# Performance work log

Hardware: AMD Instinct MI355X
Metric: run time of the kernel (lower is better)

Reference implementation:

```python
import jax, jax.numpy as jnp
import numpy as np

N_USERS = 50000
N_ENTITIES = 100000
N_RELATIONS = 16
N_EDGES = 3200000
NNZ = 2500000
CH = 64
N_HOPS = 2


def l2_normalize(x, eps=1e-12):
    # matches torch F.normalize(dim=1): x / max(||x||_2, eps)
    n = jnp.sqrt(jnp.sum(x * x, axis=-1, keepdims=True))
    return x / jnp.maximum(n, eps)


def setup_inputs() -> dict:
    key = jax.random.key(0)
    ks = jax.random.split(key, 10)
    user_emb = jax.random.normal(ks[0], (N_USERS, CH), dtype=jnp.float32)
    entity_emb = jax.random.normal(ks[1], (N_ENTITIES, CH), dtype=jnp.float32)
    weight = jax.random.normal(ks[2], (N_RELATIONS, CH), dtype=jnp.float32)
    triplet_mask = jax.random.uniform(ks[3], (N_EDGES,), dtype=jnp.float32)
    interact_vals = jnp.ones((NNZ,), dtype=jnp.float32)
    edge_head = jax.random.randint(ks[4], (N_EDGES,), 0, N_ENTITIES, dtype=jnp.int32)
    edge_tail = jax.random.randint(ks[5], (N_EDGES,), 0, N_ENTITIES, dtype=jnp.int32)
    edge_type = jax.random.randint(ks[6], (N_EDGES,), 1, N_RELATIONS + 1, dtype=jnp.int32)
    interact_rows = jax.random.randint(ks[7], (NNZ,), 0, N_USERS, dtype=jnp.int32)
    interact_cols = jax.random.randint(ks[8], (NNZ,), 0, N_ENTITIES, dtype=jnp.int32)
    return {
        'user_emb': user_emb, 'entity_emb': entity_emb, 'weight': weight,
        'triplet_mask': triplet_mask, 'interact_vals': interact_vals,
        'edge_head': edge_head, 'edge_tail': edge_tail, 'edge_type': edge_type,
        'interact_rows': interact_rows, 'interact_cols': interact_cols,
    }


def reference(user_emb, entity_emb, weight, triplet_mask, interact_vals,
              edge_head, edge_tail, edge_type, interact_rows, interact_cols):
    unmask = triplet_mask
    entity_res = entity_emb
    user_res = user_emb
    for _ in range(N_HOPS):
        # KG aggregate: gather tail embeddings, mask + relation multiply, scatter-sum to heads
        neigh = entity_emb[edge_tail] * unmask[:, None] * weight[edge_type - 1]  # [E, CH]
        entity_agg = jax.ops.segment_sum(neigh, edge_head, num_segments=N_ENTITIES)
        # user aggregate: sparse interact_mat @ entity_emb (COO gather + segment_sum)
        user_agg = jax.ops.segment_sum(
            interact_vals[:, None] * entity_emb[interact_cols],
            interact_rows, num_segments=N_USERS)
        # mess_dropout disabled (eval mode -> identity)
        entity_emb = l2_normalize(entity_agg)
        user_emb = l2_normalize(user_agg)
        entity_res = entity_res + entity_emb
        user_res = user_res + user_emb
    return entity_res, user_res
```

## Files before the change

kernel.cpp:

```cpp
#include <hip/hip_runtime.h>

#define N_USERS 50000
#define N_ENTITIES 100000
#define N_RELATIONS 16
#define N_EDGES 3200000
#define NNZ 2500000
#define CH 64

#define RPB 64
#define NB_E 1563
#define NB_U 782
#define CAP_E 2560
#define CAP_U 3840

#define BKG 128
#define BU  96
#define BTOT (BKG + BU)

__device__ __forceinline__ unsigned short f2bf(float f) {
    unsigned u = __float_as_uint(f);
    u += 0x7FFF + ((u >> 16) & 1);
    return (unsigned short)(u >> 16);
}

__global__ void __launch_bounds__(1024)
build_kernel(const float4* __restrict__ user_emb,
             const float4* __restrict__ entity_emb,
             ushort4* __restrict__ cur_bf,
             float4* __restrict__ out_entity,
             float4* __restrict__ out_user,
             const int* __restrict__ head, const int* __restrict__ tail,
             const int* __restrict__ type, const float* __restrict__ maskp,
             const int* __restrict__ irows, const int* __restrict__ icols,
             const float* __restrict__ ivals,
             int* __restrict__ cntE, int2* __restrict__ binE,
             int* __restrict__ cntU, int2* __restrict__ binU) {
    __shared__ int hist[NB_E];
    __shared__ int lbase[NB_E];
    const int blk = blockIdx.x;
    const int t = threadIdx.x;

    if (blk >= BTOT) {
        const int ne4 = N_ENTITIES * CH / 4;
        const int nu4 = N_USERS * CH / 4;
        int i = (blk - BTOT) * 1024 + t;
        if (i < ne4) {
            float4 v = entity_emb[i];
            out_entity[i] = v;
            ushort4 bq;
            bq.x = f2bf(v.x); bq.y = f2bf(v.y); bq.z = f2bf(v.z); bq.w = f2bf(v.w);
            cur_bf[i] = bq;
        }
        if (i < nu4) out_user[i] = user_emb[i];
        return;
    }

    if (blk < BKG) {
        for (int i = t; i < NB_E; i += 1024) hist[i] = 0;
        __syncthreads();
        const int chunk = (N_EDGES + BKG - 1) / BKG;
        int base = blk * chunk;
        int lim = min(base + chunk, N_EDGES);
        for (int i = base + t; i < lim; i += 1024)
            atomicAdd(&hist[head[i] >> 6], 1);
        __syncthreads();
        for (int i = t; i < NB_E; i += 1024) {
            int c = hist[i];
            lbase[i] = c ? atomicAdd(&cntE[i], c) : 0;
            hist[i] = 0;
        }
        __syncthreads();
        int i = base + t;
        for (; i + 3072 < lim; i += 4096) {
            int i0 = i, i1 = i + 1024, i2 = i + 2048, i3 = i + 3072;
            int h0 = head[i0], h1 = head[i1], h2 = head[i2], h3 = head[i3];
            int k0 = tail[i0] | ((type[i0] - 1) << 17) | ((h0 & 63) << 21);
            int k1 = tail[i1] | ((type[i1] - 1) << 17) | ((h1 & 63) << 21);
            int k2 = tail[i2] | ((type[i2] - 1) << 17) | ((h2 & 63) << 21);
            int k3 = tail[i3] | ((type[i3] - 1) << 17) | ((h3 & 63) << 21);
            float m0 = maskp[i0], m1 = maskp[i1], m2 = maskp[i2], m3 = maskp[i3];
            int b0 = h0 >> 6, b1 = h1 >> 6, b2 = h2 >> 6, b3 = h3 >> 6;
            int l0 = lbase[b0] + atomicAdd(&hist[b0], 1);
            int l1 = lbase[b1] + atomicAdd(&hist[b1], 1);
            int l2 = lbase[b2] + atomicAdd(&hist[b2], 1);
            int l3 = lbase[b3] + atomicAdd(&hist[b3], 1);
            if (l0 < CAP_E) binE[(size_t)b0 * CAP_E + l0] = make_int2(k0, __float_as_int(m0));
            if (l1 < CAP_E) binE[(size_t)b1 * CAP_E + l1] = make_int2(k1, __float_as_int(m1));
            if (l2 < CAP_E) binE[(size_t)b2 * CAP_E + l2] = make_int2(k2, __float_as_int(m2));
            if (l3 < CAP_E) binE[(size_t)b3 * CAP_E + l3] = make_int2(k3, __float_as_int(m3));
        }
        for (; i < lim; i += 1024) {
            int h = head[i];
            int b = h >> 6;
            int loc = lbase[b] + atomicAdd(&hist[b], 1);
            if (loc < CAP_E)
                binE[(size_t)b * CAP_E + loc] =
                    make_int2(tail[i] | ((type[i] - 1) << 17) | ((h & 63) << 21),
                              __float_as_int(maskp[i]));
        }
    } else {
        const int ub = blk - BKG;
        for (int i = t; i < NB_U; i += 1024) hist[i] = 0;
        __syncthreads();
        const int chunk = (NNZ + BU - 1) / BU;
        int base = ub * chunk;
        int lim = min(base + chunk, NNZ);
        for (int i = base + t; i < lim; i += 1024)
            atomicAdd(&hist[irows[i] >> 6], 1);
        __syncthreads();
        for (int i = t; i < NB_U; i += 1024) {
            int c = hist[i];
            lbase[i] = c ? atomicAdd(&cntU[i], c) : 0;
            hist[i] = 0;
        }
        __syncthreads();
        int i = base + t;
        for (; i + 3072 < lim; i += 4096) {
            int i0 = i, i1 = i + 1024, i2 = i + 2048, i3 = i + 3072;
            int r0 = irows[i0], r1 = irows[i1], r2 = irows[i2], r3 = irows[i3];
            int k0 = icols[i0] | ((r0 & 63) << 17);
            int k1 = icols[i1] | ((r1 & 63) << 17);
            int k2 = icols[i2] | ((r2 & 63) << 17);
            int k3 = icols[i3] | ((r3 & 63) << 17);
            float v0 = ivals[i0], v1 = ivals[i1], v2 = ivals[i2], v3 = ivals[i3];
            int b0 = r0 >> 6, b1 = r1 >> 6, b2 = r2 >> 6, b3 = r3 >> 6;
            int l0 = lbase[b0] + atomicAdd(&hist[b0], 1);
            int l1 = lbase[b1] + atomicAdd(&hist[b1], 1);
            int l2 = lbase[b2] + atomicAdd(&hist[b2], 1);
            int l3 = lbase[b3] + atomicAdd(&hist[b3], 1);
            if (l0 < CAP_U) binU[(size_t)b0 * CAP_U + l0] = make_int2(k0, __float_as_int(v0));
            if (l1 < CAP_U) binU[(size_t)b1 * CAP_U + l1] = make_int2(k1, __float_as_int(v1));
            if (l2 < CAP_U) binU[(size_t)b2 * CAP_U + l2] = make_int2(k2, __float_as_int(v2));
            if (l3 < CAP_U) binU[(size_t)b3 * CAP_U + l3] = make_int2(k3, __float_as_int(v3));
        }
        for (; i < lim; i += 1024) {
            int r = irows[i];
            int b = r >> 6;
            int loc = lbase[b] + atomicAdd(&hist[b], 1);
            if (loc < CAP_U)
                binU[(size_t)b * CAP_U + loc] =
                    make_int2(icols[i] | ((r & 63) << 17), __float_as_int(ivals[i]));
        }
    }
}

__global__ void __launch_bounds__(512)
sort_kernel(int2* __restrict__ binE, const int* __restrict__ cntE,
            int2* __restrict__ binU, const int* __restrict__ cntU,
            int* __restrict__ rowptr) {
    __shared__ int2 buf[CAP_U];
    __shared__ int2 sbuf[CAP_U];
    __shared__ int  hist[RPB];
    __shared__ int  offs[RPB + 1];

    const int b = blockIdx.x;
    const int t = threadIdx.x;
    const bool is_user = (b < NB_U);
    const int eb = b - NB_U;
    int2* __restrict__ bin = is_user ? (binU + (size_t)b * CAP_U)
                                     : (binE + (size_t)eb * CAP_E);
    const int cnt = is_user ? min(cntU[b], CAP_U) : min(cntE[eb], CAP_E);
    const int rsh = is_user ? 17 : 21;

    if (t < RPB) hist[t] = 0;
    for (int i = t; i < cnt; i += 512) buf[i] = bin[i];
    __syncthreads();
    for (int i = t; i < cnt; i += 512)
        atomicAdd(&hist[(buf[i].x >> rsh) & 63], 1);
    __syncthreads();
    if (t < 64) {
        int v = hist[t];
        int s = v;
        #pragma unroll
        for (int d = 1; d < 64; d <<= 1) {
            int nb = __shfl_up(s, d, 64);
            if (t >= d) s += nb;
        }
        offs[t] = s - v;
        if (t == 63) offs[64] = s;
    }
    __syncthreads();
    if (t < RPB) hist[t] = 0;
    __syncthreads();
    for (int i = t; i < cnt; i += 512) {
        int2 p = buf[i];
        int r = (p.x >> rsh) & 63;
        int k = atomicAdd(&hist[r], 1);
        sbuf[offs[r] + k] = p;
    }
    __syncthreads();
    for (int i = t; i < cnt; i += 512) bin[i] = sbuf[i];
    if (t <= 64) rowptr[b * 65 + t] = offs[t];
}

__global__ void __launch_bounds__(512)
agg_kernel(const uint2* __restrict__ cur64,
           const float* __restrict__ weight,
           const int2* __restrict__ binE, const int2* __restrict__ binU,
           const int* __restrict__ rowptr,
           unsigned short* __restrict__ nxt,
           float* __restrict__ res_e, float* __restrict__ res_u) {
    __shared__ float4 wl4[N_RELATIONS * 16];
    __shared__ int    srp[RPB + 1];

    const int b = blockIdx.x;
    const int t = threadIdx.x;
    const int w = t >> 6;
    const int lane = t & 63;
    const int g = lane >> 4;
    const int c2 = lane & 15;
    const bool is_user = (b < NB_U);
    const int eb = b - NB_U;
    const int2* __restrict__ bin = is_user ? (binU + (size_t)b * CAP_U)
                                           : (binE + (size_t)eb * CAP_E);

    if (!is_user)
        for (int i = t; i < N_RELATIONS * 16; i += 512)
            wl4[i] = ((const float4*)weight)[i];
    if (t < RPB + 1) srp[t] = rowptr[b * 65 + t];
    __syncthreads();

    #pragma unroll
    for (int rr = 0; rr < 8; ++rr) {
        const int row = (w << 3) + rr;
        const int s = srp[row], e = srp[row + 1];
        float x0 = 0.f, x1 = 0.f, x2 = 0.f, x3 = 0.f;
        int i = s;
        if (is_user) {
            for (; i + 7 < e; i += 8) {
                int2 pa = bin[i + g];
                int2 pb = bin[i + 4 + g];
                uint2 qa = cur64[(size_t)(pa.x & 0x1FFFF) * 16 + c2];
                uint2 qb = cur64[(size_t)(pb.x & 0x1FFFF) * 16 + c2];
                float sa = __int_as_float(pa.y);
                float sb = __int_as_float(pb.y);
                x0 += __uint_as_float(qa.x << 16) * sa;
                x1 += __uint_as_float(qa.x & 0xFFFF0000u) * sa;
                x2 += __uint_as_float(qa.y << 16) * sa;
                x3 += __uint_as_float(qa.y & 0xFFFF0000u) * sa;
                x0 += __uint_as_float(qb.x << 16) * sb;
                x1 += __uint_as_float(qb.x & 0xFFFF0000u) * sb;
                x2 += __uint_as_float(qb.y << 16) * sb;
                x3 += __uint_as_float(qb.y & 0xFFFF0000u) * sb;
            }
            for (; i < e; i += 4) {
                int idx = i + g;
                bool vld = idx < e;
                int2 p = bin[vld ? idx : i];
                uint2 q = cur64[(size_t)(p.x & 0x1FFFF) * 16 + c2];
                float sv = vld ? __int_as_float(p.y) : 0.f;
                x0 += __uint_as_float(q.x << 16) * sv;
                x1 += __uint_as_float(q.x & 0xFFFF0000u) * sv;
                x2 += __uint_as_float(q.y << 16) * sv;
                x3 += __uint_as_float(q.y & 0xFFFF0000u) * sv;
            }
        } else {
            for (; i + 7 < e; i += 8) {
                int2 pa = bin[i + g];
                int2 pb = bin[i + 4 + g];
                uint2 qa = cur64[(size_t)(pa.x & 0x1FFFF) * 16 + c2];
                uint2 qb = cur64[(size_t)(pb.x & 0x1FFFF) * 16 + c2];
                float4 wa = wl4[((pa.x >> 17) & 15) * 16 + c2];
                float4 wb = wl4[((pb.x >> 17) & 15) * 16 + c2];
                float sa = __int_as_float(pa.y);
                float sb = __int_as_float(pb.y);
                x0 += __uint_as_float(qa.x << 16) * (sa * wa.x);
                x1 += __uint_as_float(qa.x & 0xFFFF0000u) * (sa * wa.y);
                x2 += __uint_as_float(qa.y << 16) * (sa * wa.z);
                x3 += __uint_as_float(qa.y & 0xFFFF0000u) * (sa * wa.w);
                x0 += __uint_as_float(qb.x << 16) * (sb * wb.x);
                x1 += __uint_as_float(qb.x & 0xFFFF0000u) * (sb * wb.y);
                x2 += __uint_as_float(qb.y << 16) * (sb * wb.z);
                x3 += __uint_as_float(qb.y & 0xFFFF0000u) * (sb * wb.w);
            }
            for (; i < e; i += 4) {
                int idx = i + g;
                bool vld = idx < e;
                int2 p = bin[vld ? idx : i];
                uint2 q = cur64[(size_t)(p.x & 0x1FFFF) * 16 + c2];
                float4 wv = wl4[((p.x >> 17) & 15) * 16 + c2];
                float sv = vld ? __int_as_float(p.y) : 0.f;
                x0 += __uint_as_float(q.x << 16) * (sv * wv.x);
                x1 += __uint_as_float(q.x & 0xFFFF0000u) * (sv * wv.y);
                x2 += __uint_as_float(q.y << 16) * (sv * wv.z);
                x3 += __uint_as_float(q.y & 0xFFFF0000u) * (sv * wv.w);
            }
        }

        x0 += __shfl_xor(x0, 16, 64); x0 += __shfl_xor(x0, 32, 64);
        x1 += __shfl_xor(x1, 16, 64); x1 += __shfl_xor(x1, 32, 64);
        x2 += __shfl_xor(x2, 16, 64); x2 += __shfl_xor(x2, 32, 64);
        x3 += __shfl_xor(x3, 16, 64); x3 += __shfl_xor(x3, 32, 64);
        float ss = x0 * x0 + x1 * x1 + x2 * x2 + x3 * x3;
        #pragma unroll
        for (int o = 8; o; o >>= 1) ss += __shfl_xor(ss, o, 64);
        float inv = 1.f / fmaxf(sqrtf(ss), 1e-12f);
        float y0 = x0 * inv, y1 = x1 * inv, y2 = x2 * inv, y3 = x3 * inv;
        if (g == 0) {
            if (is_user) {
                int grow = b * RPB + row;
                if (grow < N_USERS) {
                    float4* p = (float4*)res_u + (size_t)grow * 16 + c2;
                    float4 v = *p;
                    v.x += y0; v.y += y1; v.z += y2; v.w += y3;
                    *p = v;
                }
            } else {
                int grow = eb * RPB + row;
                if (grow < N_ENTITIES) {
                    uint2 pk;
                    pk.x = (unsigned)f2bf(y0) | ((unsigned)f2bf(y1) << 16);
                    pk.y = (unsigned)f2bf(y2) | ((unsigned)f2bf(y3) << 16);
                    ((uint2*)nxt)[(size_t)grow * 16 + c2] = pk;
                    float4* p = (float4*)res_e + (size_t)grow * 16 + c2;
                    float4 v = *p;
                    v.x += y0; v.y += y1; v.z += y2; v.w += y3;
                    *p = v;
                }
            }
        }
    }
}

extern "C" void kernel_launch(void* const* d_in, const int* in_sizes, int n_in,
                              void* d_out, int out_size, void* d_ws, size_t ws_size,
                              hipStream_t stream) {
    const float* user_emb   = (const float*)d_in[0];
    const float* entity_emb = (const float*)d_in[1];
    const float* weight     = (const float*)d_in[2];
    const float* mask       = (const float*)d_in[3];
    const float* ivals      = (const float*)d_in[4];
    const int*   edge_head  = (const int*)d_in[5];
    const int*   edge_tail  = (const int*)d_in[6];
    const int*   edge_type  = (const int*)d_in[7];
    const int*   irows      = (const int*)d_in[8];
    const int*   icols      = (const int*)d_in[9];

    float* out_entity = (float*)d_out;
    float* out_user   = (float*)d_out + (size_t)N_ENTITIES * CH;

    unsigned short* curA = (unsigned short*)d_ws;
    unsigned short* curB = curA + (size_t)N_ENTITIES * CH;
    int2* binE = (int2*)(curB + (size_t)N_ENTITIES * CH);
    int2* binU = binE + (size_t)NB_E * CAP_E;
    int*  cntE = (int*)(binU + (size_t)NB_U * CAP_U);
    int*  cntU = cntE + NB_E;
    int*  rowptr = cntU + NB_U;

    hipMemsetAsync(cntE, 0, (size_t)(NB_E + NB_U) * sizeof(int), stream);
    {
        const int init_blocks = (N_ENTITIES * CH / 4 + 1023) / 1024;
        build_kernel<<<BTOT + init_blocks, 1024, 0, stream>>>(
            (const float4*)user_emb, (const float4*)entity_emb,
            (ushort4*)curA, (float4*)out_entity, (float4*)out_user,
            edge_head, edge_tail, edge_type, mask,
            irows, icols, ivals,
            cntE, binE, cntU, binU);
    }

    sort_kernel<<<NB_U + NB_E, 512, 0, stream>>>(binE, cntE, binU, cntU, rowptr);

    agg_kernel<<<NB_U + NB_E, 512, 0, stream>>>(
        (const uint2*)curA, weight, binE, binU, rowptr,
        curB, out_entity, out_user);
    agg_kernel<<<NB_U + NB_E, 512, 0, stream>>>(
        (const uint2*)curB, weight, binE, binU, rowptr,
        curA, out_entity, out_user);
}
```

Before: 550.7 us.

## Replace single-pass padded binning with two-level radix partition into compact bins

The one-pass scatter into 64-row padded bins, which uses shared histograms of up to 1563 entries and many scattered write targets, is replaced by a two-level partition. The first pass scatters into coarse 2048-row buckets, using the output buffer as scratch. A scan over the fine counts then sets offsets, and a second pass scatters into a compact contiguous array. This aims for more local writes and higher occupancy during binning, and removes the padding slack in later reads, at the cost of extra kernel launches and one more pass over the edge data.

```diff
diff --git a/kernel.cpp b/kernel.cpp
--- a/kernel.cpp
+++ b/kernel.cpp
@@ -10,12 +10,19 @@
 #define RPB 64
 #define NB_E 1563
 #define NB_U 782
-#define CAP_E 2560
-#define CAP_U 3840
-
-#define BKG 128
-#define BU  96
-#define BTOT (BKG + BU)
+#define NBUCKETS (NB_E + NB_U)
+#define STAGE 3840
+
+#define NCE 49
+#define NCU 25
+#define CAPC_E 67072
+#define CAPC_U 104448
+#define NCU_DOUT 14
+
+#define PA_KG 256
+#define PA_U  192
+#define SE 10
+#define SU 16
 
 __device__ __forceinline__ unsigned short f2bf(float f) {
     unsigned u = __float_as_uint(f);
@@ -23,27 +30,232 @@
     return (unsigned short)(u >> 16);
 }
 
+__device__ __forceinline__ int wave_incl_scan(int v, int lane) {
+    int s = v;
+    #pragma unroll
+    for (int d = 1; d < 64; d <<= 1) {
+        int x = __shfl_up(s, d, 64);
+        if (lane >= d) s += x;
+    }
+    return s;
+}
+
 __global__ void __launch_bounds__(1024)
-build_kernel(const float4* __restrict__ user_emb,
-             const float4* __restrict__ entity_emb,
-             ushort4* __restrict__ cur_bf,
-             float4* __restrict__ out_entity,
-             float4* __restrict__ out_user,
-             const int* __restrict__ head, const int* __restrict__ tail,
+passA_kernel(const int* __restrict__ head, const int* __restrict__ tail,
              const int* __restrict__ type, const float* __restrict__ maskp,
              const int* __restrict__ irows, const int* __restrict__ icols,
              const float* __restrict__ ivals,
-             int* __restrict__ cntE, int2* __restrict__ binE,
-             int* __restrict__ cntU, int2* __restrict__ binU) {
-    __shared__ int hist[NB_E];
-    __shared__ int lbase[NB_E];
+             int* __restrict__ fineCnt, int* __restrict__ cCurE,
+             int* __restrict__ cCurU,
+             int2* __restrict__ cbE, int2* __restrict__ cbU_d,
+             int2* __restrict__ cbU_w) {
+    __shared__ int histF[NB_E];
+    __shared__ int histC[64];
+    __shared__ int lbase[64];
+    __shared__ int2* utab[NCU];
     const int blk = blockIdx.x;
     const int t = threadIdx.x;
 
-    if (blk >= BTOT) {
+    if (blk < PA_KG) {
+        for (int i = t; i < NB_E; i += 1024) histF[i] = 0;
+        if (t < NCE) histC[t] = 0;
+        __syncthreads();
+        const int chunk = (N_EDGES + PA_KG - 1) / PA_KG;
+        int base = blk * chunk, lim = min(base + chunk, N_EDGES);
+        for (int i = base + t; i < lim; i += 1024) {
+            int h = head[i];
+            atomicAdd(&histF[h >> 6], 1);
+            atomicAdd(&histC[h >> 11], 1);
+        }
+        __syncthreads();
+        for (int i = t; i < NB_E; i += 1024)
+            if (histF[i]) atomicAdd(&fineCnt[NB_U + i], histF[i]);
+        if (t < NCE) {
+            int c = histC[t];
+            lbase[t] = c ? atomicAdd(&cCurE[t], c) : 0;
+            histC[t] = 0;
+        }
+        __syncthreads();
+        int i = base + t;
+        for (; i + 3072 < lim; i += 4096) {
+            int i0 = i, i1 = i + 1024, i2 = i + 2048, i3 = i + 3072;
+            int h0 = head[i0], h1 = head[i1], h2 = head[i2], h3 = head[i3];
+            int x0 = tail[i0] | ((type[i0] - 1) << 17) | ((h0 & 63) << 21) | (((h0 >> 6) & 31) << 27);
+            int x1 = tail[i1] | ((type[i1] - 1) << 17) | ((h1 & 63) << 21) | (((h1 >> 6) & 31) << 27);
+            int x2 = tail[i2] | ((type[i2] - 1) << 17) | ((h2 & 63) << 21) | (((h2 >> 6) & 31) << 27);
+            int x3 = tail[i3] | ((type[i3] - 1) << 17) | ((h3 & 63) << 21) | (((h3 >> 6) & 31) << 27);
+            float m0 = maskp[i0], m1 = maskp[i1], m2 = maskp[i2], m3 = maskp[i3];
+            int c0 = h0 >> 11, c1 = h1 >> 11, c2 = h2 >> 11, c3 = h3 >> 11;
+            int l0 = lbase[c0] + atomicAdd(&histC[c0], 1);
+            int l1 = lbase[c1] + atomicAdd(&histC[c1], 1);
+            int l2 = lbase[c2] + atomicAdd(&histC[c2], 1);
+            int l3 = lbase[c3] + atomicAdd(&histC[c3], 1);
+            if (l0 < CAPC_E) cbE[(size_t)c0 * CAPC_E + l0] = make_int2(x0, __float_as_int(m0));
+            if (l1 < CAPC_E) cbE[(size_t)c1 * CAPC_E + l1] = make_int2(x1, __float_as_int(m1));
+            if (l2 < CAPC_E) cbE[(size_t)c2 * CAPC_E + l2] = make_int2(x2, __float_as_int(m2));
+            if (l3 < CAPC_E) cbE[(size_t)c3 * CAPC_E + l3] = make_int2(x3, __float_as_int(m3));
+        }
+        for (; i < lim; i += 1024) {
+            int h = head[i];
+            int x = tail[i] | ((type[i] - 1) << 17) | ((h & 63) << 21) | (((h >> 6) & 31) << 27);
+            int c = h >> 11;
+            int loc = lbase[c] + atomicAdd(&histC[c], 1);
+            if (loc < CAPC_E)
+                cbE[(size_t)c * CAPC_E + loc] = make_int2(x, __float_as_int(maskp[i]));
+        }
+    } else {
+        if (t < NCU)
+            utab[t] = (t < NCU_DOUT) ? (cbU_d + (size_t)t * CAPC_U)
+                                     : (cbU_w + (size_t)(t - NCU_DOUT) * CAPC_U);
+        for (int i = t; i < NB_U; i += 1024) histF[i] = 0;
+        if (t < NCU) histC[t] = 0;
+        __syncthreads();
+        const int ub = blk - PA_KG;
+        const int chunk = (NNZ + PA_U - 1) / PA_U;
+        int base = ub * chunk, lim = min(base + chunk, NNZ);
+        for (int i = base + t; i < lim; i += 1024) {
+            int r = irows[i];
+            atomicAdd(&histF[r >> 6], 1);
+            atomicAdd(&histC[r >> 11], 1);
+        }
+        __syncthreads();
+        for (int i = t; i < NB_U; i += 1024)
+            if (histF[i]) atomicAdd(&fineCnt[i], histF[i]);
+        if (t < NCU) {
+            int c = histC[t];
+            lbase[t] = c ? atomicAdd(&cCurU[t], c) : 0;
+            histC[t] = 0;
+        }
+        __syncthreads();
+        int i = base + t;
+        for (; i + 3072 < lim; i += 4096) {
+            int i0 = i, i1 = i + 1024, i2 = i + 2048, i3 = i + 3072;
+            int r0 = irows[i0], r1 = irows[i1], r2 = irows[i2], r3 = irows[i3];
+            int x0 = icols[i0] | ((r0 & 63) << 17) | (((r0 >> 6) & 31) << 27);
+            int x1 = icols[i1] | ((r1 & 63) << 17) | (((r1 >> 6) & 31) << 27);
+            int x2 = icols[i2] | ((r2 & 63) << 17) | (((r2 >> 6) & 31) << 27);
+            int x3 = icols[i3] | ((r3 & 63) << 17) | (((r3 >> 6) & 31) << 27);
+            float v0 = ivals[i0], v1 = ivals[i1], v2 = ivals[i2], v3 = ivals[i3];
+            int c0 = r0 >> 11, c1 = r1 >> 11, c2 = r2 >> 11, c3 = r3 >> 11;
+            int l0 = lbase[c0] + atomicAdd(&histC[c0], 1);
+            int l1 = lbase[c1] + atomicAdd(&histC[c1], 1);
+            int l2 = lbase[c2] + atomicAdd(&histC[c2], 1);
+            int l3 = lbase[c3] + atomicAdd(&histC[c3], 1);
+            if (l0 < CAPC_U) utab[c0][l0] = make_int2(x0, __float_as_int(v0));
+            if (l1 < CAPC_U) utab[c1][l1] = make_int2(x1, __float_as_int(v1));
+            if (l2 < CAPC_U) utab[c2][l2] = make_int2(x2, __float_as_int(v2));
+            if (l3 < CAPC_U) utab[c3][l3] = make_int2(x3, __float_as_int(v3));
+        }
+        for (; i < lim; i += 1024) {
+            int r = irows[i];
+            int x = icols[i] | ((r & 63) << 17) | (((r >> 6) & 31) << 27);
+            int c = r >> 11;
+            int loc = lbase[c] + atomicAdd(&histC[c], 1);
+            if (loc < CAPC_U) utab[c][loc] = make_int2(x, __float_as_int(ivals[i]));
+        }
+    }
+}
+
+__global__ void __launch_bounds__(512)
+scan_kernel(const int* __restrict__ fineCnt, int* __restrict__ fineBase,
+            int* __restrict__ fineCur) {
+    __shared__ int wsums[8];
+    __shared__ int carry_s;
+    const int t = threadIdx.x, w = t >> 6, lane = t & 63;
+    if (t == 0) carry_s = 0;
+    __syncthreads();
+    for (int base = 0; base < NBUCKETS; base += 512) {
+        int i = base + t;
+        int v = (i < NBUCKETS) ? fineCnt[i] : 0;
+        int s = wave_incl_scan(v, lane);
+        if (lane == 63) wsums[w] = s;
+        __syncthreads();
+        int carry = carry_s;
+        if (w == 0) {
+            int ws = (lane < 8) ? wsums[lane] : 0;
+            int ss = wave_incl_scan(ws, lane);
+            if (lane < 8) wsums[lane] = ss - ws;
+        }
+        __syncthreads();
+        int excl = s - v + wsums[w] + carry;
+        if (i < NBUCKETS) { fineBase[i] = excl; fineCur[i] = excl; }
+        __syncthreads();
+        if (t == 511) carry_s = excl + v;
+        __syncthreads();
+    }
+}
+
+__global__ void __launch_bounds__(1024)
+passB_kernel(const int* __restrict__ cCurE, const int* __restrict__ cCurU,
+             const int2* __restrict__ cbE, const int2* __restrict__ cbU_d,
+             const int2* __restrict__ cbU_w,
+             int* __restrict__ fineCur, int2* __restrict__ binAll) {
+    __shared__ int h32[32];
+    __shared__ int lb[32];
+    const int blk = blockIdx.x, t = threadIdx.x;
+    const int2* __restrict__ src;
+    int cnt, sub, S, fid0;
+    if (blk < NCE * SE) {
+        int c = blk / SE; sub = blk % SE; S = SE;
+        cnt = min(cCurE[c], CAPC_E);
+        src = cbE + (size_t)c * CAPC_E;
+        fid0 = NB_U + c * 32;
+    } else {
+        int c = (blk - NCE * SE) / SU; sub = (blk - NCE * SE) % SU; S = SU;
+        cnt = min(cCurU[c], CAPC_U);
+        src = (c < NCU_DOUT) ? cbU_d + (size_t)c * CAPC_U
+                             : cbU_w + (size_t)(c - NCU_DOUT) * CAPC_U;
+        fid0 = c * 32;
+    }
+    int len = (cnt + S - 1) / S;
+    int b0 = sub * len, b1 = min(b0 + len, cnt);
+    if (t < 32) h32[t] = 0;
+    __syncthreads();
+    for (int i = b0 + t; i < b1; i += 1024)
+        atomicAdd(&h32[(src[i].x >> 27) & 31], 1);
+    __syncthreads();
+    if (t < 32) {
+        int c2 = h32[t];
+        lb[t] = c2 ? atomicAdd(&fineCur[fid0 + t], c2) : 0;
+        h32[t] = 0;
+    }
+    __syncthreads();
+    int i = b0 + t;
+    for (; i + 3072 < b1; i += 4096) {
+        int2 e0 = src[i], e1 = src[i + 1024], e2 = src[i + 2048], e3 = src[i + 3072];
+        int f0 = (e0.x >> 27) & 31, f1 = (e1.x >> 27) & 31;
+        int f2 = (e2.x >> 27) & 31, f3 = (e3.x >> 27) & 31;
+        int l0 = lb[f0] + atomicAdd(&h32[f0], 1);
+        int l1 = lb[f1] + atomicAdd(&h32[f1], 1);
+        int l2 = lb[f2] + atomicAdd(&h32[f2], 1);
+        int l3 = lb[f3] + atomicAdd(&h32[f3], 1);
+        binAll[l0] = e0; binAll[l1] = e1; binAll[l2] = e2; binAll[l3] = e3;
+    }
+    for (; i < b1; i += 1024) {
+        int2 e = src[i];
+        int f = (e.x >> 27) & 31;
+        binAll[lb[f] + atomicAdd(&h32[f], 1)] = e;
+    }
+}
+
+__global__ void __launch_bounds__(512)
+sortinit_kernel(int2* __restrict__ binAll, const int* __restrict__ fineCnt,
+                const int* __restrict__ fineBase, int* __restrict__ rowptr,
+                const float4* __restrict__ user_emb,
+                const float4* __restrict__ entity_emb,
+                ushort4* __restrict__ cur_bf,
+                float4* __restrict__ out_entity, float4* __restrict__ out_user) {
+    __shared__ int2 buf[STAGE];
+    __shared__ int2 sbuf[STAGE];
+    __shared__ int  hist[RPB];
+    __shared__ int  offs[RPB + 1];
+
+    const int blk = blockIdx.x;
+    const int t = threadIdx.x;
+    if (blk >= NBUCKETS) {
         const int ne4 = N_ENTITIES * CH / 4;
         const int nu4 = N_USERS * CH / 4;
-        int i = (blk - BTOT) * 1024 + t;
+        int i = (blk - NBUCKETS) * 512 + t;
         if (i < ne4) {
             float4 v = entity_emb[i];
             out_entity[i] = v;
@@ -55,111 +267,11 @@
         return;
     }
 
-    if (blk < BKG) {
-        for (int i = t; i < NB_E; i += 1024) hist[i] = 0;
-        __syncthreads();
-        const int chunk = (N_EDGES + BKG - 1) / BKG;
-        int base = blk * chunk;
-        int lim = min(base + chunk, N_EDGES);
-        for (int i = base + t; i < lim; i += 1024)
-            atomicAdd(&hist[head[i] >> 6], 1);
-        __syncthreads();
-        for (int i = t; i < NB_E; i += 1024) {
-            int c = hist[i];
-            lbase[i] = c ? atomicAdd(&cntE[i], c) : 0;
-            hist[i] = 0;
-        }
-        __syncthreads();
-        int i = base + t;
-        for (; i + 3072 < lim; i += 4096) {
-            int i0 = i, i1 = i + 1024, i2 = i + 2048, i3 = i + 3072;
-            int h0 = head[i0], h1 = head[i1], h2 = head[i2], h3 = head[i3];
-            int k0 = tail[i0] | ((type[i0] - 1) << 17) | ((h0 & 63) << 21);
-            int k1 = tail[i1] | ((type[i1] - 1) << 17) | ((h1 & 63) << 21);
-            int k2 = tail[i2] | ((type[i2] - 1) << 17) | ((h2 & 63) << 21);
-            int k3 = tail[i3] | ((type[i3] - 1) << 17) | ((h3 & 63) << 21);
-            float m0 = maskp[i0], m1 = maskp[i1], m2 = maskp[i2], m3 = maskp[i3];
-            int b0 = h0 >> 6, b1 = h1 >> 6, b2 = h2 >> 6, b3 = h3 >> 6;
-            int l0 = lbase[b0] + atomicAdd(&hist[b0], 1);
-            int l1 = lbase[b1] + atomicAdd(&hist[b1], 1);
-            int l2 = lbase[b2] + atomicAdd(&hist[b2], 1);
-            int l3 = lbase[b3] + atomicAdd(&hist[b3], 1);
-            if (l0 < CAP_E) binE[(size_t)b0 * CAP_E + l0] = make_int2(k0, __float_as_int(m0));
-            if (l1 < CAP_E) binE[(size_t)b1 * CAP_E + l1] = make_int2(k1, __float_as_int(m1));
-            if (l2 < CAP_E) binE[(size_t)b2 * CAP_E + l2] = make_int2(k2, __float_as_int(m2));
-            if (l3 < CAP_E) binE[(size_t)b3 * CAP_E + l3] = make_int2(k3, __float_as_int(m3));
-        }
-        for (; i < lim; i += 1024) {
-            int h = head[i];
-            int b = h >> 6;
-            int loc = lbase[b] + atomicAdd(&hist[b], 1);
-            if (loc < CAP_E)
-                binE[(size_t)b * CAP_E + loc] =
-                    make_int2(tail[i] | ((type[i] - 1) << 17) | ((h & 63) << 21),
-                              __float_as_int(maskp[i]));
-        }
-    } else {
-        const int ub = blk - BKG;
-        for (int i = t; i < NB_U; i += 1024) hist[i] = 0;
-        __syncthreads();
-        const int chunk = (NNZ + BU - 1) / BU;
-        int base = ub * chunk;
-        int lim = min(base + chunk, NNZ);
-        for (int i = base + t; i < lim; i += 1024)
-            atomicAdd(&hist[irows[i] >> 6], 1);
-        __syncthreads();
-        for (int i = t; i < NB_U; i += 1024) {
-            int c = hist[i];
-            lbase[i] = c ? atomicAdd(&cntU[i], c) : 0;
-            hist[i] = 0;
-        }
-        __syncthreads();
-        int i = base + t;
-        for (; i + 3072 < lim; i += 4096) {
-            int i0 = i, i1 = i + 1024, i2 = i + 2048, i3 = i + 3072;
-            int r0 = irows[i0], r1 = irows[i1], r2 = irows[i2], r3 = irows[i3];
-            int k0 = icols[i0] | ((r0 & 63) << 17);
-            int k1 = icols[i1] | ((r1 & 63) << 17);
-            int k2 = icols[i2] | ((r2 & 63) << 17);
-            int k3 = icols[i3] | ((r3 & 63) << 17);
-            float v0 = ivals[i0], v1 = ivals[i1], v2 = ivals[i2], v3 = ivals[i3];
-            int b0 = r0 >> 6, b1 = r1 >> 6, b2 = r2 >> 6, b3 = r3 >> 6;
-            int l0 = lbase[b0] + atomicAdd(&hist[b0], 1);
-            int l1 = lbase[b1] + atomicAdd(&hist[b1], 1);
-            int l2 = lbase[b2] + atomicAdd(&hist[b2], 1);
-            int l3 = lbase[b3] + atomicAdd(&hist[b3], 1);
-            if (l0 < CAP_U) binU[(size_t)b0 * CAP_U + l0] = make_int2(k0, __float_as_int(v0));
-            if (l1 < CAP_U) binU[(size_t)b1 * CAP_U + l1] = make_int2(k1, __float_as_int(v1));
-            if (l2 < CAP_U) binU[(size_t)b2 * CAP_U + l2] = make_int2(k2, __float_as_int(v2));
-            if (l3 < CAP_U) binU[(size_t)b3 * CAP_U + l3] = make_int2(k3, __float_as_int(v3));
-        }
-        for (; i < lim; i += 1024) {
-            int r = irows[i];
-            int b = r >> 6;
-            int loc = lbase[b] + atomicAdd(&hist[b], 1);
-            if (loc < CAP_U)
-                binU[(size_t)b * CAP_U + loc] =
-                    make_int2(icols[i] | ((r & 63) << 17), __float_as_int(ivals[i]));
-        }
-    }
-}
-
-__global__ void __launch_bounds__(512)
-sort_kernel(int2* __restrict__ binE, const int* __restrict__ cntE,
-            int2* __restrict__ binU, const int* __restrict__ cntU,
-            int* __restrict__ rowptr) {
-    __shared__ int2 buf[CAP_U];
-    __shared__ int2 sbuf[CAP_U];
-    __shared__ int  hist[RPB];
-    __shared__ int  offs[RPB + 1];
-
-    const int b = blockIdx.x;
-    const int t = threadIdx.x;
+    const int b = blk;
     const bool is_user = (b < NB_U);
-    const int eb = b - NB_U;
-    int2* __restrict__ bin = is_user ? (binU + (size_t)b * CAP_U)
-                                     : (binE + (size_t)eb * CAP_E);
-    const int cnt = is_user ? min(cntU[b], CAP_U) : min(cntE[eb], CAP_E);
+    const int base = fineBase[b];
+    int2* __restrict__ bin = binAll + base;
+    const int cnt = min(fineCnt[b], STAGE);
     const int rsh = is_user ? 17 : 21;
 
     if (t < RPB) hist[t] = 0;
@@ -170,12 +282,7 @@
     __syncthreads();
     if (t < 64) {
         int v = hist[t];
-        int s = v;
-        #pragma unroll
-        for (int d = 1; d < 64; d <<= 1) {
-            int nb = __shfl_up(s, d, 64);
-            if (t >= d) s += nb;
-        }
+        int s = wave_incl_scan(v, t);
         offs[t] = s - v;
         if (t == 63) offs[64] = s;
     }
@@ -190,14 +297,13 @@
     }
     __syncthreads();
     for (int i = t; i < cnt; i += 512) bin[i] = sbuf[i];
-    if (t <= 64) rowptr[b * 65 + t] = offs[t];
+    if (t <= 64) rowptr[b * 65 + t] = base + offs[t];
 }
 
 __global__ void __launch_bounds__(512)
 agg_kernel(const uint2* __restrict__ cur64,
            const float* __restrict__ weight,
-           const int2* __restrict__ binE, const int2* __restrict__ binU,
-           const int* __restrict__ rowptr,
+           const int2* __restrict__ binAll, const int* __restrict__ rowptr,
            unsigned short* __restrict__ nxt,
            float* __restrict__ res_e, float* __restrict__ res_u) {
     __shared__ float4 wl4[N_RELATIONS * 16];
@@ -211,8 +317,6 @@
     const int c2 = lane & 15;
     const bool is_user = (b < NB_U);
     const int eb = b - NB_U;
-    const int2* __restrict__ bin = is_user ? (binU + (size_t)b * CAP_U)
-                                           : (binE + (size_t)eb * CAP_E);
 
     if (!is_user)
         for (int i = t; i < N_RELATIONS * 16; i += 512)
@@ -228,8 +332,8 @@
         int i = s;
         if (is_user) {
             for (; i + 7 < e; i += 8) {
-                int2 pa = bin[i + g];
-                int2 pb = bin[i + 4 + g];
+                int2 pa = binAll[i + g];
+                int2 pb = binAll[i + 4 + g];
                 uint2 qa = cur64[(size_t)(pa.x & 0x1FFFF) * 16 + c2];
                 uint2 qb = cur64[(size_t)(pb.x & 0x1FFFF) * 16 + c2];
                 float sa = __int_as_float(pa.y);
@@ -246,7 +350,7 @@
             for (; i < e; i += 4) {
                 int idx = i + g;
                 bool vld = idx < e;
-                int2 p = bin[vld ? idx : i];
+                int2 p = binAll[vld ? idx : i];
                 uint2 q = cur64[(size_t)(p.x & 0x1FFFF) * 16 + c2];
                 float sv = vld ? __int_as_float(p.y) : 0.f;
                 x0 += __uint_as_float(q.x << 16) * sv;
@@ -256,8 +360,8 @@
             }
         } else {
             for (; i + 7 < e; i += 8) {
-                int2 pa = bin[i + g];
-                int2 pb = bin[i + 4 + g];
+                int2 pa = binAll[i + g];
+                int2 pb = binAll[i + 4 + g];
                 uint2 qa = cur64[(size_t)(pa.x & 0x1FFFF) * 16 + c2];
                 uint2 qb = cur64[(size_t)(pb.x & 0x1FFFF) * 16 + c2];
                 float4 wa = wl4[((pa.x >> 17) & 15) * 16 + c2];
@@ -276,7 +380,7 @@
             for (; i < e; i += 4) {
                 int idx = i + g;
                 bool vld = idx < e;
-                int2 p = bin[vld ? idx : i];
+                int2 p = binAll[vld ? idx : i];
                 uint2 q = cur64[(size_t)(p.x & 0x1FFFF) * 16 + c2];
                 float4 wv = wl4[((p.x >> 17) & 15) * 16 + c2];
                 float sv = vld ? __int_as_float(p.y) : 0.f;
@@ -339,31 +443,43 @@
     float* out_entity = (float*)d_out;
     float* out_user   = (float*)d_out + (size_t)N_ENTITIES * CH;
 
+    int2* cbE   = (int2*)d_out;
+    int2* cbU_d = cbE + (size_t)NCE * CAPC_E;
+
     unsigned short* curA = (unsigned short*)d_ws;
     unsigned short* curB = curA + (size_t)N_ENTITIES * CH;
-    int2* binE = (int2*)(curB + (size_t)N_ENTITIES * CH);
-    int2* binU = binE + (size_t)NB_E * CAP_E;
-    int*  cntE = (int*)(binU + (size_t)NB_U * CAP_U);
-    int*  cntU = cntE + NB_E;
-    int*  rowptr = cntU + NB_U;
-
-    hipMemsetAsync(cntE, 0, (size_t)(NB_E + NB_U) * sizeof(int), stream);
+    int2* binAll = (int2*)(curB + (size_t)N_ENTITIES * CH);
+    int2* cbU_w  = binAll + (size_t)(N_EDGES + NNZ);
+    int*  fineCnt  = (int*)(cbU_w + (size_t)(NCU - NCU_DOUT) * CAPC_U);
+    int*  cCurE    = fineCnt + NBUCKETS;
+    int*  cCurU    = cCurE + NCE;
+    int*  fineBase = cCurU + NCU;
+    int*  fineCur  = fineBase + NBUCKETS;
+    int*  rowptr   = fineCur + NBUCKETS;
+
+    hipMemsetAsync(fineCnt, 0, (size_t)(NBUCKETS + NCE + NCU) * sizeof(int), stream);
+
+    passA_kernel<<<PA_KG + PA_U, 1024, 0, stream>>>(
+        edge_head, edge_tail, edge_type, mask, irows, icols, ivals,
+        fineCnt, cCurE, cCurU, cbE, cbU_d, cbU_w);
+
+    scan_kernel<<<1, 512, 0, stream>>>(fineCnt, fineBase, fineCur);
+
+    passB_kernel<<<NCE * SE + NCU * SU, 1024, 0, stream>>>(
+        cCurE, cCurU, cbE, cbU_d, cbU_w, fineCur, binAll);
+
     {
-        const int init_blocks = (N_ENTITIES * CH / 4 + 1023) / 1024;
-        build_kernel<<<BTOT + init_blocks, 1024, 0, stream>>>(
+        const int init_blocks = (N_ENTITIES * CH / 4 + 511) / 512;
+        sortinit_kernel<<<NBUCKETS + init_blocks, 512, 0, stream>>>(
+            binAll, fineCnt, fineBase, rowptr,
             (const float4*)user_emb, (const float4*)entity_emb,
-            (ushort4*)curA, (float4*)out_entity, (float4*)out_user,
-            edge_head, edge_tail, edge_type, mask,
-            irows, icols, ivals,
-            cntE, binE, cntU, binU);
-    }
-
-    sort_kernel<<<NB_U + NB_E, 512, 0, stream>>>(binE, cntE, binU, cntU, rowptr);
-
-    agg_kernel<<<NB_U + NB_E, 512, 0, stream>>>(
-        (const uint2*)curA, weight, binE, binU, rowptr,
+            (ushort4*)curA, (float4*)out_entity, (float4*)out_user);
+    }
+
+    agg_kernel<<<NBUCKETS, 512, 0, stream>>>(
+        (const uint2*)curA, weight, binAll, rowptr,
         curB, out_entity, out_user);
-    agg_kernel<<<NB_U + NB_E, 512, 0, stream>>>(
-        (const uint2*)curB, weight, binE, binU, rowptr,
+    agg_kernel<<<NBUCKETS, 512, 0, stream>>>(
+        (const uint2*)curB, weight, binAll, rowptr,
         curA, out_entity, out_user);
 }
```

Result: faster. 522.1 us (-5.2%).
